# Kernel tuning notes

Hardware: AMD Instinct MI355X
Metric: run time of the kernel (lower is better)

The kernel has to match this reference:

```python
import jax, jax.numpy as jnp
import numpy as np

H_IMG, W_IMG = 16, 64
HK, WK = 7, 11
DIM, NUM_HEADS = 384, 8
BATCH = 32
SEQ = H_IMG * W_IMG  # 1024


def build_local_mask():
    # Faithful to the torch constructor: for each query position (i,j), a
    # (hk x wk) window of zeros in a padded canvas; everything else -inf.
    h, w, hk, wk = H_IMG, W_IMG, HK, WK
    mask = np.ones((h * w, h + hk - 1, w + wk - 1), dtype=np.float32)
    for i in range(h):
        for j in range(w):
            mask[w * i + j, i:i + hk, j:j + wk] = 0.0
    mask_c = mask[:, hk // 2:h + hk // 2, wk // 2:w + wk // 2].reshape(h * w, h * w)
    out = np.where(mask_c == 1.0, np.float32(-np.inf), mask_c).astype(np.float32)
    return jnp.asarray(out)  # [S, S]


def setup_inputs() -> dict:
    key = jax.random.key(0)
    k1, k2, k3, k4 = jax.random.split(key, 4)
    s = 1.0 / np.sqrt(DIM)
    return {
        "x": jax.random.normal(k1, (BATCH, SEQ, DIM), dtype=jnp.float32),
        "w_qkv": jax.random.normal(k2, (DIM, 3 * DIM), dtype=jnp.float32) * s,
        "w_proj": jax.random.normal(k3, (DIM, DIM), dtype=jnp.float32) * s,
        "b_proj": jax.random.normal(k4, (DIM,), dtype=jnp.float32) * 0.01,
        "mask": build_local_mask(),
    }


def reference(x, w_qkv, w_proj, b_proj, mask):
    B, S, C = x.shape
    H = NUM_HEADS
    D = C // H
    scale = D ** -0.5
    qkv = (x @ w_qkv).reshape(B, S, 3, H, D)
    qkv = jnp.transpose(qkv, (2, 0, 3, 1, 4))  # [3, B, H, S, D]
    q, k, v = qkv[0] * scale, qkv[1], qkv[2]
    attn = jnp.einsum("bhsd,bhtd->bhst", q, k)  # [B, H, S, S]
    attn = attn + mask[None, None]               # additive local-window bias
    attn = jax.nn.softmax(attn, axis=-1)
    out = jnp.einsum("bhst,bhtd->bhsd", attn, v)
    out = jnp.transpose(out, (0, 2, 1, 3)).reshape(B, S, C)
    return out @ w_proj + b_proj
```

## Files before the change

### kernel.cpp

```cpp
#include <hip/hip_runtime.h>
#include <hip/hip_bf16.h>


typedef __attribute__((ext_vector_type(8))) unsigned short ushort8;
typedef __attribute__((ext_vector_type(4))) unsigned short ushort4v;
typedef __attribute__((ext_vector_type(8))) short short8v;
typedef __attribute__((ext_vector_type(4))) float floatx4;

__device__ __forceinline__ float bf2f(unsigned short u) {
  union { unsigned int i; float f; } x;
  x.i = ((unsigned int)u) << 16;
  return x.f;
}

__device__ __forceinline__ unsigned short f2bu(float f) {
  union { float f; unsigned int i; } x;
  x.f = f;
  unsigned int lsb = (x.i >> 16) & 1u;
  x.i += 0x7FFFu + lsb;
  return (unsigned short)(x.i >> 16);
}

__device__ __forceinline__ void gload_lds16(const void* g, void* l) {
  __builtin_amdgcn_global_load_lds(
      (const __attribute__((address_space(1))) unsigned int*)g,
      (__attribute__((address_space(3))) unsigned int*)l, 16, 0, 0);
}

__global__ __launch_bounds__(256) void cvt_f32_bf16(
    const float4* __restrict__ in, ushort4v* __restrict__ out, int n4) {
  const int i = blockIdx.x * 256 + threadIdx.x;
  if (i < n4) {
    const float4 v = in[i];
    ushort4v o;
    o[0] = f2bu(v.x); o[1] = f2bu(v.y); o[2] = f2bu(v.z); o[3] = f2bu(v.w);
    out[i] = o;
  }
}

__global__ __launch_bounds__(256) void transpose_cvt(
    const float* __restrict__ in, unsigned short* __restrict__ out, int R, int C) {
  __shared__ float t[32][33];
  const int c0 = blockIdx.x * 32, r0 = blockIdx.y * 32;
  const int tx = threadIdx.x, ty = threadIdx.y;
  #pragma unroll
  for (int rr = ty; rr < 32; rr += 8) t[rr][tx] = in[(size_t)(r0 + rr) * C + c0 + tx];
  __syncthreads();
  #pragma unroll
  for (int rr = ty; rr < 32; rr += 8)
    out[(size_t)(c0 + rr) * R + r0 + tx] = f2bu(t[tx][rr]);
}

template <int MODE>
__global__ __launch_bounds__(512) void gemm_mfma(
    const unsigned short* __restrict__ A,
    const unsigned short* __restrict__ Bt,
    const float* __restrict__ bias, float* __restrict__ outf,
    unsigned short* __restrict__ qws, unsigned short* __restrict__ kws,
    unsigned short* __restrict__ vtws)
{
  __shared__ unsigned short smem[32768];
  const int tid = threadIdx.x;
  const int lane = tid & 63, w = tid >> 6;
  const int wm = w & 3, wn = w >> 2;

  const int nbx = gridDim.x;
  const int nwg = nbx * gridDim.y;
  const int bid = blockIdx.y * nbx + blockIdx.x;
  const int swz = (bid & 7) * (nwg >> 3) + (bid >> 3);
  const int n0 = (swz % nbx) * 128;
  const int m0 = (swz / nbx) * 128;

  floatx4 acc[2][4];
  #pragma unroll
  for (int mi = 0; mi < 2; ++mi)
    #pragma unroll
    for (int ni = 0; ni < 4; ++ni)
      acc[mi][ni] = (floatx4){0.f, 0.f, 0.f, 0.f};

  const int srow = tid >> 2;
  const int kslot16 = (tid & 3) * 16;

  auto ASB = [&](int buf) -> char* { return (char*)smem + buf * 8192; };
  auto BSB = [&](int buf) -> char* { return (char*)smem + 32768 + buf * 8192; };

  auto STAGE = [&](int buf, int k0) {
    const int kb = kslot16 ^ ((srow & 3) << 4);
    gload_lds16((const char*)A + (size_t)(m0 + srow) * 768 + k0 * 2 + kb,
                ASB(buf) + w * 1024);
    gload_lds16((const char*)Bt + (size_t)(n0 + srow) * 768 + k0 * 2 + kb,
                BSB(buf) + w * 1024);
  };

  auto COMPUTE = [&](int buf) {
    short8v a[2], b[4];
    const int kgb = (lane >> 4) * 16;
    #pragma unroll
    for (int mi = 0; mi < 2; ++mi) {
      const int r = wm * 32 + mi * 16 + (lane & 15);
      a[mi] = *reinterpret_cast<const short8v*>(
          ASB(buf) + r * 64 + (kgb ^ ((r & 3) << 4)));
    }
    #pragma unroll
    for (int ni = 0; ni < 4; ++ni) {
      const int r = wn * 64 + ni * 16 + (lane & 15);
      b[ni] = *reinterpret_cast<const short8v*>(
          BSB(buf) + r * 64 + (kgb ^ ((r & 3) << 4)));
    }
    #pragma unroll
    for (int mi = 0; mi < 2; ++mi)
      #pragma unroll
      for (int ni = 0; ni < 4; ++ni)
        acc[mi][ni] = __builtin_amdgcn_mfma_f32_16x16x32_bf16(
            a[mi], b[ni], acc[mi][ni], 0, 0, 0);
  };

  STAGE(0, 0);
  STAGE(1, 32);

  #pragma unroll
  for (int s = 0; s < 6; ++s) {
    const int rb = (s & 1) * 2;
    const int sb = rb ^ 2;
    if (s < 5) {
      STAGE(sb, (2 * s + 2) * 32);
      STAGE(sb + 1, (2 * s + 3) * 32);
      asm volatile("s_waitcnt vmcnt(4)" ::: "memory");
    } else {
      asm volatile("s_waitcnt vmcnt(0)" ::: "memory");
    }
    __builtin_amdgcn_s_barrier();
    __builtin_amdgcn_s_setprio(1);
    COMPUTE(rb);
    COMPUTE(rb + 1);
    __builtin_amdgcn_s_setprio(0);
    asm volatile("s_waitcnt lgkmcnt(0)" ::: "memory");
    __builtin_amdgcn_s_barrier();
  }

  const int col_l = lane & 15;
  const int row_l = (lane >> 4) * 4;

  if (MODE == 0) {
    const float QSCALE = 0.14433756729740643f;
    const int which = n0 / 384;
    if (which < 2) {
      unsigned short* dstb = (which == 0) ? qws : kws;
      const float scale = (which == 0) ? QSCALE : 1.f;
      #pragma unroll
      for (int ni = 0; ni < 4; ++ni) {
        const int cg = n0 + wn * 64 + ni * 16 + col_l;
        const int rem = cg - which * 384;
        const int h = rem / 48;
        const int d = rem - h * 48;
        #pragma unroll
        for (int mi = 0; mi < 2; ++mi) {
          #pragma unroll
          for (int reg = 0; reg < 4; ++reg) {
            const int r = m0 + wm * 32 + mi * 16 + row_l + reg;
            const int bb = r >> 10, s = r & 1023;
            dstb[(((size_t)(bb * 8 + h)) * 1024 + s) * 48 + d] =
                f2bu(acc[mi][ni][reg] * scale);
          }
        }
      }
    } else {
      unsigned short* T = smem;
      #pragma unroll
      for (int ni = 0; ni < 4; ++ni) {
        const int col = wn * 64 + ni * 16 + col_l;
        #pragma unroll
        for (int mi = 0; mi < 2; ++mi) {
          const int rowb = wm * 32 + mi * 16 + row_l;
          #pragma unroll
          for (int reg = 0; reg < 4; ++reg)
            T[col * 136 + rowb + reg] = f2bu(acc[mi][ni][reg]);
        }
      }
      __syncthreads();
      const int col = tid >> 2, q = tid & 3;
      const int cg = n0 + col;
      const int rem = cg - 768;
      const int h = rem / 48, d = rem - h * 48;
      const int bb = m0 >> 10;
      const int s0 = (m0 & 1023) + q * 32;
      unsigned short* dst =
          vtws + (((size_t)(bb * 8 + h)) * 48 + d) * 1024 + s0;
      const unsigned short* src = T + col * 136 + q * 32;
      #pragma unroll
      for (int j = 0; j < 4; ++j)
        *reinterpret_cast<ushort8*>(dst + j * 8) =
            *reinterpret_cast<const ushort8*>(src + j * 8);
    }
  } else {
    #pragma unroll
    for (int ni = 0; ni < 4; ++ni) {
      const int cg = n0 + wn * 64 + ni * 16 + col_l;
      const float bv = bias[cg];
      #pragma unroll
      for (int mi = 0; mi < 2; ++mi) {
        #pragma unroll
        for (int reg = 0; reg < 4; ++reg) {
          const int r = m0 + wm * 32 + mi * 16 + row_l + reg;
          outf[(size_t)r * 384 + cg] = acc[mi][ni][reg] + bv;
        }
      }
    }
  }
}

__global__ __launch_bounds__(256) void attn_mfma(
    const unsigned short* __restrict__ qws,
    const unsigned short* __restrict__ kws,
    const unsigned short* __restrict__ vt,
    unsigned short* __restrict__ attn_out)
{
  __shared__ unsigned short plds_all[4 * 64 * 72];

  const int tid = threadIdx.x;
  const int w = tid >> 6;
  const int lane = tid & 63;
  const int blk = blockIdx.x;
  const int sw = ((blk & 7) << 7) | (blk >> 3);
  const int task = sw * 4 + w;
  const int i  = task & 15;
  const int bh = task >> 4;
  const int ql = lane & 15;
  const int g  = lane >> 4;

  unsigned short* plds = plds_all + w * 4608;

  {
    const uint4 zz = make_uint4(0, 0, 0, 0);
    #pragma unroll
    for (int z = 0; z < 9; ++z)
      reinterpret_cast<uint4*>(plds)[lane + z * 64] = zz;
  }

  const unsigned short* qbase = qws + (size_t)bh * 1024 * 48;
  const unsigned short* kbase = kws + (size_t)bh * 1024 * 48;
  const unsigned short* vbase = vt  + (size_t)bh * 48 * 1024;

  const short8v zfrag = (short8v){0, 0, 0, 0, 0, 0, 0, 0};

  short8v qf[4][2];
  #pragma unroll
  for (int qt = 0; qt < 4; ++qt) {
    const unsigned short* qrow = qbase + (size_t)(i * 64 + qt * 16 + ql) * 48;
    qf[qt][0] = *reinterpret_cast<const short8v*>(qrow + 8 * g);
    qf[qt][1] = (g < 2) ? *reinterpret_cast<const short8v*>(qrow + 32 + 8 * g)
                        : zfrag;
  }

  floatx4 ot[3][4];
  #pragma unroll
  for (int dt = 0; dt < 3; ++dt)
    #pragma unroll
    for (int qt = 0; qt < 4; ++qt)
      ot[dt][qt] = (floatx4){0.f, 0.f, 0.f, 0.f};
  float mreg[4] = {-INFINITY, -INFINITY, -INFINITY, -INFINITY};
  float lreg[4] = {0.f, 0.f, 0.f, 0.f};

  const int ki0 = (i - 3 < 0) ? 0 : i - 3;
  const int ki1 = (i + 3 > 15) ? 15 : i + 3;

  for (int ki = ki0; ki <= ki1; ++ki) {
    short8v kf[4][2];
    #pragma unroll
    for (int kt = 0; kt < 4; ++kt) {
      const unsigned short* krow = kbase + (size_t)(ki * 64 + kt * 16 + ql) * 48;
      kf[kt][0] = *reinterpret_cast<const short8v*>(krow + 8 * g);
      kf[kt][1] = (g < 2) ? *reinterpret_cast<const short8v*>(krow + 32 + 8 * g)
                          : zfrag;
    }
    short8v vf[3][2];
    #pragma unroll
    for (int dt = 0; dt < 3; ++dt)
      #pragma unroll
      for (int c = 0; c < 2; ++c)
        vf[dt][c] = *reinterpret_cast<const short8v*>(
            vbase + (size_t)(16 * dt + ql) * 1024 + ki * 64 + 32 * c + 8 * g);

    #pragma unroll
    for (int qt = 0; qt < 4; ++qt) {
      const int kts = (qt == 0) ? 0 : qt - 1;
      const int kte = (qt == 3) ? 3 : qt + 1;
      floatx4 s[4];
      #pragma unroll
      for (int kt = 0; kt < 4; ++kt) {
        if (kt < kts || kt > kte) continue;
        s[kt] = __builtin_amdgcn_mfma_f32_16x16x32_bf16(
            kf[kt][0], qf[qt][0], (floatx4){0.f, 0.f, 0.f, 0.f}, 0, 0, 0);
        s[kt] = __builtin_amdgcn_mfma_f32_16x16x32_bf16(
            kf[kt][1], qf[qt][1], s[kt], 0, 0, 0);
      }
      const int qcol = qt * 16 + ql;
      float pmax = -INFINITY;
      #pragma unroll
      for (int kt = 0; kt < 4; ++kt) {
        if (kt < kts || kt > kte) continue;
        #pragma unroll
        for (int r = 0; r < 4; ++r) {
          const int delta = kt * 16 + 4 * g + r - qcol;
          const bool ok = (delta <= 5) && (delta >= -5);
          s[kt][r] = ok ? s[kt][r] : -INFINITY;
          pmax = fmaxf(pmax, s[kt][r]);
        }
      }
      if (!__all(pmax - mreg[qt] <= 8.0f)) {
        float mt = fmaxf(pmax, __shfl_xor(pmax, 16, 64));
        mt = fmaxf(mt, __shfl_xor(mt, 32, 64));
        const float mnew = fmaxf(mreg[qt], mt);
        const float corr = __expf(mreg[qt] - mnew);
        lreg[qt] *= corr;
        #pragma unroll
        for (int dt = 0; dt < 3; ++dt) {
          ot[dt][qt][0] *= corr; ot[dt][qt][1] *= corr;
          ot[dt][qt][2] *= corr; ot[dt][qt][3] *= corr;
        }
        mreg[qt] = mnew;
      }
      float ps = 0.f;
      #pragma unroll
      for (int kt = 0; kt < 4; ++kt) {
        if (kt < kts || kt > kte) continue;
        #pragma unroll
        for (int r = 0; r < 4; ++r) {
          const float p = __expf(s[kt][r] - mreg[qt]);
          s[kt][r] = p;
          ps += p;
        }
      }
      ps += __shfl_xor(ps, 16, 64);
      ps += __shfl_xor(ps, 32, 64);
      lreg[qt] += ps;
      #pragma unroll
      for (int kt = 0; kt < 4; ++kt) {
        if (kt < kts || kt > kte) continue;
        uint2 pk;
        pk.x = (unsigned int)f2bu(s[kt][0]) | ((unsigned int)f2bu(s[kt][1]) << 16);
        pk.y = (unsigned int)f2bu(s[kt][2]) | ((unsigned int)f2bu(s[kt][3]) << 16);
        *reinterpret_cast<uint2*>(&plds[(qt * 16 + ql) * 72 + kt * 16 + 4 * g]) = pk;
      }
    }

    __builtin_amdgcn_s_setprio(1);
    #pragma unroll
    for (int qt = 0; qt < 4; ++qt) {
      #pragma unroll
      for (int c = 0; c < 2; ++c) {
        if ((qt == 0 && c == 1) || (qt == 3 && c == 0)) continue;
        const short8v pf = *reinterpret_cast<const short8v*>(
            &plds[(qt * 16 + ql) * 72 + 32 * c + 8 * g]);
        #pragma unroll
        for (int dt = 0; dt < 3; ++dt)
          ot[dt][qt] = __builtin_amdgcn_mfma_f32_16x16x32_bf16(
              vf[dt][c], pf, ot[dt][qt], 0, 0, 0);
      }
    }
    __builtin_amdgcn_s_setprio(0);
  }

  const int b = bh >> 3, h = bh & 7;
  #pragma unroll
  for (int qt = 0; qt < 4; ++qt) {
    const float inv = 1.0f / lreg[qt];
    unsigned short* orow =
        attn_out + (size_t)(b * 1024 + i * 64 + qt * 16 + ql) * 384 + h * 48;
    #pragma unroll
    for (int dt = 0; dt < 3; ++dt) {
      const int d0 = 16 * dt + 4 * g;
      unsigned int w0 = (unsigned int)f2bu(ot[dt][qt][0] * inv) |
                        ((unsigned int)f2bu(ot[dt][qt][1] * inv) << 16);
      unsigned int w1 = (unsigned int)f2bu(ot[dt][qt][2] * inv) |
                        ((unsigned int)f2bu(ot[dt][qt][3] * inv) << 16);
      *reinterpret_cast<unsigned int*>(orow + d0)     = w0;
      *reinterpret_cast<unsigned int*>(orow + d0 + 2) = w1;
    }
  }
}

extern "C" void kernel_launch(void* const* d_in, const int* in_sizes, int n_in,
                              void* d_out, int out_size, void* d_ws, size_t ws_size,
                              hipStream_t stream) {
  const float* x      = (const float*)d_in[0];
  const float* w_qkv  = (const float*)d_in[1];
  const float* w_proj = (const float*)d_in[2];
  const float* b_proj = (const float*)d_in[3];

  const size_t T = 25165824;
  char* ws = (char*)d_ws;
  unsigned short* xb    = (unsigned short*)ws;
  unsigned short* qws   = (unsigned short*)(ws + T);
  unsigned short* kws   = (unsigned short*)(ws + 2 * T);
  unsigned short* vtws  = (unsigned short*)(ws + 3 * T);
  unsigned short* wqkvT = (unsigned short*)(ws + 4 * T);
  unsigned short* wpT   = (unsigned short*)(ws + 4 * T + 884736);
  unsigned short* attn_out = xb;
  float* out = (float*)d_out;

  cvt_f32_bf16<<<12288, 256, 0, stream>>>((const float4*)x, (ushort4v*)xb, 3145728);
  transpose_cvt<<<dim3(36, 12), dim3(32, 8), 0, stream>>>(w_qkv, wqkvT, 384, 1152);
  transpose_cvt<<<dim3(12, 12), dim3(32, 8), 0, stream>>>(w_proj, wpT, 384, 384);

  gemm_mfma<0><<<dim3(9, 256), 512, 0, stream>>>(xb, wqkvT, nullptr, nullptr,
                                                 qws, kws, vtws);
  attn_mfma<<<dim3(1024), 256, 0, stream>>>(qws, kws, vtws, attn_out);
  gemm_mfma<1><<<dim3(3, 256), 512, 0, stream>>>(attn_out, wpT, b_proj, out,
                                                 nullptr, nullptr, nullptr);
}
```

Measured before the change: 131.7 us.

## Fuse fp32-to-bf16 input conversion into QKV GEMM with register-staged A loads

Removes the separate conversion kernel that wrote a bf16 copy of x. The QKV GEMM now reads fp32 x directly into registers, converts it with packed bf16 instructions, and writes it to LDS, while B tiles still use direct global-to-LDS loads. The main loop is re-pipelined around these register banks and their wait counts. This saves one launch and a full write-then-read of x through memory. In exchange the GEMM reads twice as many A bytes and needs more registers and hand-tuned vmcnt sequencing.

```diff
diff --git a/kernel.cpp b/kernel.cpp
--- a/kernel.cpp
+++ b/kernel.cpp
@@ -3,7 +3,6 @@
 
 
 typedef __attribute__((ext_vector_type(8))) unsigned short ushort8;
-typedef __attribute__((ext_vector_type(4))) unsigned short ushort4v;
 typedef __attribute__((ext_vector_type(8))) short short8v;
 typedef __attribute__((ext_vector_type(4))) float floatx4;
 
@@ -21,21 +20,16 @@
   return (unsigned short)(x.i >> 16);
 }
 
+__device__ __forceinline__ unsigned int cvtpk_bf16(float lo, float hi) {
+  unsigned int r;
+  asm("v_cvt_pk_bf16_f32 %0, %1, %2" : "=v"(r) : "v"(lo), "v"(hi));
+  return r;
+}
+
 __device__ __forceinline__ void gload_lds16(const void* g, void* l) {
   __builtin_amdgcn_global_load_lds(
       (const __attribute__((address_space(1))) unsigned int*)g,
       (__attribute__((address_space(3))) unsigned int*)l, 16, 0, 0);
-}
-
-__global__ __launch_bounds__(256) void cvt_f32_bf16(
-    const float4* __restrict__ in, ushort4v* __restrict__ out, int n4) {
-  const int i = blockIdx.x * 256 + threadIdx.x;
-  if (i < n4) {
-    const float4 v = in[i];
-    ushort4v o;
-    o[0] = f2bu(v.x); o[1] = f2bu(v.y); o[2] = f2bu(v.z); o[3] = f2bu(v.w);
-    out[i] = o;
-  }
 }
 
 __global__ __launch_bounds__(256) void transpose_cvt(
@@ -51,13 +45,186 @@
     out[(size_t)(c0 + rr) * R + r0 + tx] = f2bu(t[tx][rr]);
 }
 
-template <int MODE>
-__global__ __launch_bounds__(512) void gemm_mfma(
+__global__ __launch_bounds__(512) void gemm_qkv(
+    const float* __restrict__ X,
+    const unsigned short* __restrict__ Bt,
+    unsigned short* __restrict__ qws, unsigned short* __restrict__ kws,
+    unsigned short* __restrict__ vtws)
+{
+  __shared__ unsigned short smem[32768];
+  const int tid = threadIdx.x;
+  const int lane = tid & 63, w = tid >> 6;
+  const int wm = w & 3, wn = w >> 2;
+
+  const int nbx = gridDim.x;
+  const int nwg = nbx * gridDim.y;
+  const int bid = blockIdx.y * nbx + blockIdx.x;
+  const int swz = (bid & 7) * (nwg >> 3) + (bid >> 3);
+  const int n0 = (swz % nbx) * 128;
+  const int m0 = (swz / nbx) * 128;
+
+  floatx4 acc[2][4];
+  #pragma unroll
+  for (int mi = 0; mi < 2; ++mi)
+    #pragma unroll
+    for (int ni = 0; ni < 4; ++ni)
+      acc[mi][ni] = (floatx4){0.f, 0.f, 0.f, 0.f};
+
+  const int arow = tid >> 2;
+  const int aslot = tid & 3;
+  const int adst = arow * 64 + ((aslot * 16) ^ ((arow & 3) << 4));
+  const float* asrc = X + (size_t)(m0 + arow) * 384 + aslot * 8;
+
+  auto ASB = [&](int buf) -> char* { return (char*)smem + buf * 8192; };
+  auto BSB = [&](int buf) -> char* { return (char*)smem + 32768 + buf * 8192; };
+
+  float4 bank0[4], bank1[4];
+
+  auto LOADA = [&](float4* bank, int p) {
+    #pragma unroll
+    for (int tile = 0; tile < 2; ++tile) {
+      const float* s = asrc + (p * 2 + tile) * 32;
+      bank[tile * 2 + 0] = *reinterpret_cast<const float4*>(s);
+      bank[tile * 2 + 1] = *reinterpret_cast<const float4*>(s + 4);
+    }
+  };
+  auto DSWRITE = [&](const float4* bank, int p) {
+    #pragma unroll
+    for (int tile = 0; tile < 2; ++tile) {
+      const float4 f0 = bank[tile * 2 + 0];
+      const float4 f1 = bank[tile * 2 + 1];
+      uint4 v;
+      v.x = cvtpk_bf16(f0.x, f0.y); v.y = cvtpk_bf16(f0.z, f0.w);
+      v.z = cvtpk_bf16(f1.x, f1.y); v.w = cvtpk_bf16(f1.z, f1.w);
+      *reinterpret_cast<uint4*>(ASB(2 * (p & 1) + tile) + adst) = v;
+    }
+  };
+  const int srow = tid >> 2;
+  const int kslot16 = (tid & 3) * 16;
+  auto BGLOAD = [&](int p) {
+    #pragma unroll
+    for (int tile = 0; tile < 2; ++tile) {
+      const int t = p * 2 + tile;
+      const int kb = kslot16 ^ ((srow & 3) << 4);
+      gload_lds16((const char*)Bt + (size_t)(n0 + srow) * 768 + t * 64 + kb,
+                  BSB(2 * (p & 1) + tile) + w * 1024);
+    }
+  };
+  auto COMPUTE = [&](int buf) {
+    short8v a[2], b[4];
+    const int kgb = (lane >> 4) * 16;
+    #pragma unroll
+    for (int mi = 0; mi < 2; ++mi) {
+      const int r = wm * 32 + mi * 16 + (lane & 15);
+      a[mi] = *reinterpret_cast<const short8v*>(
+          ASB(buf) + r * 64 + (kgb ^ ((r & 3) << 4)));
+    }
+    #pragma unroll
+    for (int ni = 0; ni < 4; ++ni) {
+      const int r = wn * 64 + ni * 16 + (lane & 15);
+      b[ni] = *reinterpret_cast<const short8v*>(
+          BSB(buf) + r * 64 + (kgb ^ ((r & 3) << 4)));
+    }
+    #pragma unroll
+    for (int mi = 0; mi < 2; ++mi)
+      #pragma unroll
+      for (int ni = 0; ni < 4; ++ni)
+        acc[mi][ni] = __builtin_amdgcn_mfma_f32_16x16x32_bf16(
+            a[mi], b[ni], acc[mi][ni], 0, 0, 0);
+  };
+
+  LOADA(bank0, 0);
+  BGLOAD(0);
+  LOADA(bank1, 1);
+  BGLOAD(1);
+  asm volatile("s_waitcnt vmcnt(8)" ::: "memory");
+  DSWRITE(bank0, 0);
+  asm volatile("s_waitcnt vmcnt(2)" ::: "memory");
+  DSWRITE(bank1, 1);
+  LOADA(bank0, 2);
+  asm volatile("s_waitcnt lgkmcnt(0)" ::: "memory");
+  __builtin_amdgcn_s_barrier();
+
+  #pragma unroll
+  for (int s = 0; s < 6; ++s) {
+    __builtin_amdgcn_s_setprio(1);
+    COMPUTE(2 * (s & 1));
+    COMPUTE(2 * (s & 1) + 1);
+    __builtin_amdgcn_s_setprio(0);
+    asm volatile("s_waitcnt lgkmcnt(0)" ::: "memory");
+    if (s + 2 <= 5) {
+      asm volatile("s_waitcnt vmcnt(4)" ::: "memory");
+    } else if (s + 1 <= 5) {
+      asm volatile("s_waitcnt vmcnt(0)" ::: "memory");
+    }
+    __builtin_amdgcn_s_barrier();
+    if (s + 2 <= 5) {
+      BGLOAD(s + 2);
+      asm volatile("s_waitcnt vmcnt(2)" ::: "memory");
+      DSWRITE((s & 1) ? bank1 : bank0, s + 2);
+      if (s + 3 <= 5) LOADA((s & 1) ? bank0 : bank1, s + 3);
+    }
+  }
+
+  const int col_l = lane & 15;
+  const int row_l = (lane >> 4) * 4;
+  const float QSCALE = 0.14433756729740643f;
+  const int which = n0 / 384;
+
+  if (which < 2) {
+    unsigned short* dstb = (which == 0) ? qws : kws;
+    const float scale = (which == 0) ? QSCALE : 1.f;
+    #pragma unroll
+    for (int ni = 0; ni < 4; ++ni) {
+      const int cg = n0 + wn * 64 + ni * 16 + col_l;
+      const int rem = cg - which * 384;
+      const int h = rem / 48;
+      const int d = rem - h * 48;
+      #pragma unroll
+      for (int mi = 0; mi < 2; ++mi) {
+        #pragma unroll
+        for (int reg = 0; reg < 4; ++reg) {
+          const int r = m0 + wm * 32 + mi * 16 + row_l + reg;
+          const int bb = r >> 10, s = r & 1023;
+          dstb[(((size_t)(bb * 8 + h)) * 1024 + s) * 48 + d] =
+              f2bu(acc[mi][ni][reg] * scale);
+        }
+      }
+    }
+  } else {
+    unsigned short* T = smem;
+    #pragma unroll
+    for (int ni = 0; ni < 4; ++ni) {
+      const int col = wn * 64 + ni * 16 + col_l;
+      #pragma unroll
+      for (int mi = 0; mi < 2; ++mi) {
+        const int rowb = wm * 32 + mi * 16 + row_l;
+        #pragma unroll
+        for (int reg = 0; reg < 4; ++reg)
+          T[col * 136 + rowb + reg] = f2bu(acc[mi][ni][reg]);
+      }
+    }
+    __syncthreads();
+    const int col = tid >> 2, q = tid & 3;
+    const int cg = n0 + col;
+    const int rem = cg - 768;
+    const int h = rem / 48, d = rem - h * 48;
+    const int bb = m0 >> 10;
+    const int s0 = (m0 & 1023) + q * 32;
+    unsigned short* dst =
+        vtws + (((size_t)(bb * 8 + h)) * 48 + d) * 1024 + s0;
+    const unsigned short* src = T + col * 136 + q * 32;
+    #pragma unroll
+    for (int j = 0; j < 4; ++j)
+      *reinterpret_cast<ushort8*>(dst + j * 8) =
+          *reinterpret_cast<const ushort8*>(src + j * 8);
+  }
+}
+
+__global__ __launch_bounds__(512) void gemm_proj(
     const unsigned short* __restrict__ A,
     const unsigned short* __restrict__ Bt,
-    const float* __restrict__ bias, float* __restrict__ outf,
-    unsigned short* __restrict__ qws, unsigned short* __restrict__ kws,
-    unsigned short* __restrict__ vtws)
+    const float* __restrict__ bias, float* __restrict__ outf)
 {
   __shared__ unsigned short smem[32768];
   const int tid = threadIdx.x;
@@ -140,70 +307,16 @@
 
   const int col_l = lane & 15;
   const int row_l = (lane >> 4) * 4;
-
-  if (MODE == 0) {
-    const float QSCALE = 0.14433756729740643f;
-    const int which = n0 / 384;
-    if (which < 2) {
-      unsigned short* dstb = (which == 0) ? qws : kws;
-      const float scale = (which == 0) ? QSCALE : 1.f;
-      #pragma unroll
-      for (int ni = 0; ni < 4; ++ni) {
-        const int cg = n0 + wn * 64 + ni * 16 + col_l;
-        const int rem = cg - which * 384;
-        const int h = rem / 48;
-        const int d = rem - h * 48;
-        #pragma unroll
-        for (int mi = 0; mi < 2; ++mi) {
-          #pragma unroll
-          for (int reg = 0; reg < 4; ++reg) {
-            const int r = m0 + wm * 32 + mi * 16 + row_l + reg;
-            const int bb = r >> 10, s = r & 1023;
-            dstb[(((size_t)(bb * 8 + h)) * 1024 + s) * 48 + d] =
-                f2bu(acc[mi][ni][reg] * scale);
-          }
-        }
-      }
-    } else {
-      unsigned short* T = smem;
-      #pragma unroll
-      for (int ni = 0; ni < 4; ++ni) {
-        const int col = wn * 64 + ni * 16 + col_l;
-        #pragma unroll
-        for (int mi = 0; mi < 2; ++mi) {
-          const int rowb = wm * 32 + mi * 16 + row_l;
-          #pragma unroll
-          for (int reg = 0; reg < 4; ++reg)
-            T[col * 136 + rowb + reg] = f2bu(acc[mi][ni][reg]);
-        }
-      }
-      __syncthreads();
-      const int col = tid >> 2, q = tid & 3;
-      const int cg = n0 + col;
-      const int rem = cg - 768;
-      const int h = rem / 48, d = rem - h * 48;
-      const int bb = m0 >> 10;
-      const int s0 = (m0 & 1023) + q * 32;
-      unsigned short* dst =
-          vtws + (((size_t)(bb * 8 + h)) * 48 + d) * 1024 + s0;
-      const unsigned short* src = T + col * 136 + q * 32;
-      #pragma unroll
-      for (int j = 0; j < 4; ++j)
-        *reinterpret_cast<ushort8*>(dst + j * 8) =
-            *reinterpret_cast<const ushort8*>(src + j * 8);
-    }
-  } else {
-    #pragma unroll
-    for (int ni = 0; ni < 4; ++ni) {
-      const int cg = n0 + wn * 64 + ni * 16 + col_l;
-      const float bv = bias[cg];
-      #pragma unroll
-      for (int mi = 0; mi < 2; ++mi) {
-        #pragma unroll
-        for (int reg = 0; reg < 4; ++reg) {
-          const int r = m0 + wm * 32 + mi * 16 + row_l + reg;
-          outf[(size_t)r * 384 + cg] = acc[mi][ni][reg] + bv;
-        }
+  #pragma unroll
+  for (int ni = 0; ni < 4; ++ni) {
+    const int cg = n0 + wn * 64 + ni * 16 + col_l;
+    const float bv = bias[cg];
+    #pragma unroll
+    for (int mi = 0; mi < 2; ++mi) {
+      #pragma unroll
+      for (int reg = 0; reg < 4; ++reg) {
+        const int r = m0 + wm * 32 + mi * 16 + row_l + reg;
+        outf[(size_t)r * 384 + cg] = acc[mi][ni][reg] + bv;
       }
     }
   }
@@ -390,22 +503,18 @@
 
   const size_t T = 25165824;
   char* ws = (char*)d_ws;
-  unsigned short* xb    = (unsigned short*)ws;
+  unsigned short* attn_out = (unsigned short*)ws;
   unsigned short* qws   = (unsigned short*)(ws + T);
   unsigned short* kws   = (unsigned short*)(ws + 2 * T);
   unsigned short* vtws  = (unsigned short*)(ws + 3 * T);
   unsigned short* wqkvT = (unsigned short*)(ws + 4 * T);
   unsigned short* wpT   = (unsigned short*)(ws + 4 * T + 884736);
-  unsigned short* attn_out = xb;
   float* out = (float*)d_out;
 
-  cvt_f32_bf16<<<12288, 256, 0, stream>>>((const float4*)x, (ushort4v*)xb, 3145728);
   transpose_cvt<<<dim3(36, 12), dim3(32, 8), 0, stream>>>(w_qkv, wqkvT, 384, 1152);
   transpose_cvt<<<dim3(12, 12), dim3(32, 8), 0, stream>>>(w_proj, wpT, 384, 384);
 
-  gemm_mfma<0><<<dim3(9, 256), 512, 0, stream>>>(xb, wqkvT, nullptr, nullptr,
-                                                 qws, kws, vtws);
+  gemm_qkv<<<dim3(9, 256), 512, 0, stream>>>(x, wqkvT, qws, kws, vtws);
   attn_mfma<<<dim3(1024), 256, 0, stream>>>(qws, kws, vtws, attn_out);
-  gemm_mfma<1><<<dim3(3, 256), 512, 0, stream>>>(attn_out, wpT, b_proj, out,
-                                                 nullptr, nullptr, nullptr);
-}
+  gemm_proj<<<dim3(3, 256), 512, 0, stream>>>(attn_out, wpT, b_proj, out);
+}
```

Result: no change. 131.0 us (-0.5%).
